# Optimization experiments

Hardware: AMD Instinct MI355X
Metric: run time of the kernel (lower is better)

Reference implementation:

```python
import jax, jax.numpy as jnp
import numpy as np

B, N, D = 8, 1024, 256
H, U = 8, 64  # num_heads, units per head


def setup_inputs() -> dict:
    key = jax.random.key(0)
    ks = jax.random.split(key, 8)
    X = jax.random.normal(ks[0], (B, N, D), dtype=jnp.float32)
    A = (jax.random.uniform(ks[1], (B, N, N)) < 0.1).astype(jnp.float32)
    A = jnp.maximum(A, jnp.eye(N, dtype=jnp.float32)[None])
    s = 1.0 / np.sqrt(D)
    kernel = jax.random.normal(ks[2], (D, H * U), dtype=jnp.float32) * s
    kernel_residual = jax.random.normal(ks[3], (D, H * U), dtype=jnp.float32) * s
    su = 1.0 / np.sqrt(U)
    attn_kernel_self = jax.random.normal(ks[4], (H, U, 1), dtype=jnp.float32) * su
    attn_kernel_neighs = jax.random.normal(ks[5], (H, U, 1), dtype=jnp.float32) * su
    bias = jnp.zeros((H * U,), dtype=jnp.float32)
    return {
        "X": X, "A": A,
        "kernel": kernel, "kernel_residual": kernel_residual,
        "attn_kernel_self": attn_kernel_self,
        "attn_kernel_neighs": attn_kernel_neighs,
        "bias": bias,
    }


def reference(X, A, kernel, kernel_residual, attn_kernel_self, attn_kernel_neighs, bias):
    # feature projections: [B,N,H*U]
    features = X @ kernel
    features_residual = X @ kernel_residual
    f = features.reshape(B, N, H, U)  # bnhu
    # additive attention logits per head
    attn_self = jnp.einsum('bnhu,hu->bnh', f, attn_kernel_self[..., 0])
    attn_neigh = jnp.einsum('bnhu,hu->bnh', f, attn_kernel_neighs[..., 0])
    dense = attn_self[:, :, None, :] + attn_neigh[:, None, :, :]  # b n k h
    dense = jax.nn.leaky_relu(dense, negative_slope=0.2)
    # mask non-edges, softmax over neighbor axis k
    dense = dense + (-1e10) * (1.0 - A)[..., None]
    attn_coef = jax.nn.softmax(dense, axis=2)
    # (dropout is identity in inference mode)
    node_features = jnp.einsum('bnkh,bkhu->bnhu', attn_coef, f)
    node_features = node_features.reshape(B, N, H * U) + features_residual + bias
    # head_reduction == 'concat' -> keep [B,N,H*U]
    return jax.nn.relu(node_features)
```

## Files before the change

### kernel.cpp

```cpp
#include <hip/hip_runtime.h>
#include <stdint.h>


typedef __attribute__((ext_vector_type(8))) short short8;
typedef __attribute__((ext_vector_type(4))) float f32x4;

__device__ __forceinline__ unsigned short f32_to_bf16(float f) {
    unsigned int u = __float_as_uint(f);
    u = (u + 0x7fffu + ((u >> 16) & 1u)) >> 16;
    return (unsigned short)u;
}
__device__ __forceinline__ float bf16_to_f32(unsigned short s) {
    return __uint_as_float(((unsigned int)s) << 16);
}
__device__ __forceinline__ void load_lds16(const unsigned short* g, unsigned short* l) {
    __builtin_amdgcn_global_load_lds(
        (const __attribute__((address_space(1))) unsigned int*)g,
        (__attribute__((address_space(3))) unsigned int*)l, 16, 0, 0);
}

__global__ __launch_bounds__(256) void pack_a(const float* __restrict__ X,
                                              unsigned short* __restrict__ Abig) {
    const int idx = blockIdx.x * 256 + threadIdx.x;
    const int m  = idx >> 6;
    const int kg = (idx & 63) << 2;
    float4 x = *(const float4*)&X[m * 256 + kg];
    const float xs[4] = {x.x, x.y, x.z, x.w};
    union { unsigned short u[4]; uint64_t q; } hq, lq;
    #pragma unroll
    for (int i = 0; i < 4; i++) {
        unsigned short h = f32_to_bf16(xs[i]);
        hq.u[i] = h;
        lq.u[i] = f32_to_bf16(xs[i] - bf16_to_f32(h));
    }
    unsigned short* r = Abig + (size_t)m * 768;
    *(uint64_t*)(r + kg)       = hq.q;
    *(uint64_t*)(r + 256 + kg) = hq.q;
    *(uint64_t*)(r + 512 + kg) = lq.q;
}

__global__ __launch_bounds__(256) void pack_b(const float* __restrict__ Wk,
                                              const float* __restrict__ Wr,
                                              unsigned short* __restrict__ Bpack) {
    const int idx = blockIdx.x * 256 + threadIdx.x;
    const int n = idx / 768;
    const int k = idx - n * 768;
    const float* __restrict__ W = (n < 512) ? Wk : Wr;
    const int nc = n & 511;
    const float w = W[(k & 255) * 512 + nc];
    unsigned short h = f32_to_bf16(w);
    unsigned short o = (k >= 256 && k < 512) ? f32_to_bf16(w - bf16_to_f32(h)) : h;
    Bpack[idx] = o;
}

__global__ __launch_bounds__(512) void attn_ck(const float* __restrict__ kernel,
                                               const float* __restrict__ aks,
                                               const float* __restrict__ akn,
                                               float* __restrict__ ck) {
    const int d = blockIdx.x, j = threadIdx.x;
    const float kv = kernel[d * 512 + j];
    float a = kv * aks[j];
    float b = kv * akn[j];
    #pragma unroll
    for (int m = 32; m; m >>= 1) { a += __shfl_xor(a, m, 64); b += __shfl_xor(b, m, 64); }
    const int lane = j & 63, h = j >> 6;
    if (lane == 0) { ck[d * 16 + h] = a; ck[d * 16 + 8 + h] = b; }
}

__global__ __launch_bounds__(256) void attn_sa(const float* __restrict__ X,
                                               const float* __restrict__ ck,
                                               float* __restrict__ saan) {
    __shared__ __align__(16) float Xs[16][260];
    __shared__ __align__(16) float ckL[4096];
    const int t = threadIdx.x, row0 = blockIdx.x * 16;
    #pragma unroll
    for (int i = 0; i < 4; i++) {
        const int q = t + i * 256;
        const int r = q >> 6, c4 = (q & 63) * 4;
        *(float4*)&Xs[r][c4] = *(const float4*)&X[(size_t)(row0 + r) * 256 + c4];
        *(float4*)&ckL[q * 4] = *(const float4*)&ck[q * 4];
    }
    __syncthreads();
    const int r = t >> 4, o = t & 15;
    float acc = 0.f;
    #pragma unroll 4
    for (int d = 0; d < 256; d++) acc = fmaf(Xs[r][d], ckL[d * 16 + o], acc);
    saan[(size_t)(row0 + r) * 16 + o] = acc;
}

#define GK 768
__global__ __launch_bounds__(256) void gemm_bf16(const unsigned short* __restrict__ Ab,
                                                 const unsigned short* __restrict__ Bp,
                                                 unsigned short* __restrict__ featT,
                                                 float* __restrict__ outr) {
    __shared__ __align__(16) unsigned short As[128 * 32];
    __shared__ __align__(16) unsigned short Bs[128 * 32];
    const int tid = threadIdx.x;
    const int lane = tid & 63, wave = tid >> 6;
    const int wr = wave >> 1, wc = wave & 1;
    const int m0 = blockIdx.x * 128, n0 = blockIdx.y * 128;
    const int l15 = lane & 15, lhi = lane >> 4;

    f32x4 acc[4][4] = {};

    for (int k0 = 0; k0 < GK; k0 += 32) {
        #pragma unroll
        for (int i = 0; i < 2; i++) {
            const int s = tid + i * 256;
            const int row = s >> 2, kc = (s & 3) * 8;
            load_lds16(Ab + (size_t)(m0 + row) * GK + k0 + kc, &As[s * 8]);
            load_lds16(Bp + (size_t)(n0 + row) * GK + k0 + kc, &Bs[s * 8]);
        }
        asm volatile("s_waitcnt vmcnt(0)" ::: "memory");
        __syncthreads();
        short8 a[4], b[4];
        #pragma unroll
        for (int mi = 0; mi < 4; mi++)
            a[mi] = *(const short8*)&As[(wr * 64 + mi * 16 + l15) * 32 + lhi * 8];
        #pragma unroll
        for (int ni = 0; ni < 4; ni++)
            b[ni] = *(const short8*)&Bs[(wc * 64 + ni * 16 + l15) * 32 + lhi * 8];
        #pragma unroll
        for (int mi = 0; mi < 4; mi++)
            #pragma unroll
            for (int ni = 0; ni < 4; ni++)
                acc[mi][ni] = __builtin_amdgcn_mfma_f32_16x16x32_bf16(a[mi], b[ni], acc[mi][ni], 0, 0, 0);
        __syncthreads();
    }

    if (n0 < 512) {
        #pragma unroll
        for (int mi = 0; mi < 4; mi++)
            #pragma unroll
            for (int ni = 0; ni < 4; ni++) {
                const int col = n0 + wc * 64 + ni * 16 + l15;
                const int rbase = m0 + wr * 64 + mi * 16 + lhi * 4;
                const int bb = rbase >> 10, nl = rbase & 1023;
                union { unsigned short u[4]; uint64_t q; } pk;
                #pragma unroll
                for (int r = 0; r < 4; r++) pk.u[r] = f32_to_bf16(acc[mi][ni][r]);
                *(uint64_t*)&featT[(size_t)bb * 524288 + (size_t)col * 1024 + nl] = pk.q;
            }
    } else {
        #pragma unroll
        for (int mi = 0; mi < 4; mi++)
            #pragma unroll
            for (int ni = 0; ni < 4; ni++) {
                const int col = (n0 - 512) + wc * 64 + ni * 16 + l15;
                const int rbase = m0 + wr * 64 + mi * 16 + lhi * 4;
                #pragma unroll
                for (int r = 0; r < 4; r++)
                    outr[(size_t)(rbase + r) * 512 + col] = acc[mi][ni][r];
            }
    }
}

__global__ __launch_bounds__(512) void gat_mfma(
    const float* __restrict__ A, const unsigned short* __restrict__ featT,
    const float* __restrict__ saan, const float* __restrict__ bias,
    float* __restrict__ out) {
    __shared__ float an_s[1024][9];
    __shared__ float A_lds[32][33];
    __shared__ float inv_lds[8][32];

    const int blk = blockIdx.x;
    const int b  = blk & 7;
    const int n0 = (blk >> 3) * 32;
    const int t = threadIdx.x;
    const int w = t >> 6;
    const int lane = t & 63;
    const int l15 = lane & 15, lhi = lane >> 4;

    #pragma unroll
    for (int i = 0; i < 4; i++) {
        const int idx = i * 512 + t;
        const int k = idx >> 1, half = (idx & 1) * 4;
        float4 v = *(const float4*)&saan[(size_t)(b * 1024 + k) * 16 + 8 + half];
        an_s[k][half + 0] = v.x; an_s[k][half + 1] = v.y;
        an_s[k][half + 2] = v.z; an_s[k][half + 3] = v.w;
    }
    float as_r[2];
    #pragma unroll
    for (int mi = 0; mi < 2; mi++)
        as_r[mi] = saan[(size_t)(b * 1024 + n0 + mi * 16 + l15) * 16 + w];

    float4 regA;
    const int sr = t >> 3, sc = (t & 7) * 4;
    if (t < 256)
        regA = *(const float4*)&A[(size_t)(b * 1024 + n0 + sr) * 1024 + sc];

    f32x4 acc[2][4] = {};
    float ps[2] = {0.f, 0.f};
    const unsigned short* __restrict__ fT = featT + (size_t)b * 524288;

    __syncthreads();

    for (int k0 = 0; k0 < 1024; k0 += 32) {
        if (t < 256) {
            A_lds[sr][sc + 0] = regA.x; A_lds[sr][sc + 1] = regA.y;
            A_lds[sr][sc + 2] = regA.z; A_lds[sr][sc + 3] = regA.w;
            if (k0 + 32 < 1024)
                regA = *(const float4*)&A[(size_t)(b * 1024 + n0 + sr) * 1024 + (k0 + 32) + sc];
        }
        __syncthreads();

        union { short8 s8; unsigned int u32[4]; } pa[2];
        #pragma unroll
        for (int mi = 0; mi < 2; mi++) {
            #pragma unroll
            for (int q = 0; q < 4; q++) {
                float pv[2];
                #pragma unroll
                for (int d = 0; d < 2; d++) {
                    const int kk = lhi * 8 + q * 2 + d;
                    float x = as_r[mi] + an_s[k0 + kk][w];
                    x = fmaxf(x, 0.2f * x);
                    const float e = __expf(x);
                    pv[d] = (A_lds[mi * 16 + l15][kk] > 0.5f) ? e : 0.f;
                }
                unsigned int pk;
                asm("v_cvt_pk_bf16_f32 %0, %1, %2" : "=v"(pk) : "v"(pv[0]), "v"(pv[1]));
                pa[mi].u32[q] = pk;
                ps[mi] += __uint_as_float(pk << 16) + __uint_as_float(pk & 0xffff0000u);
            }
        }
        short8 bf[4];
        #pragma unroll
        for (int ni = 0; ni < 4; ni++)
            bf[ni] = *(const short8*)&fT[(size_t)(w * 64 + ni * 16 + l15) * 1024 + k0 + lhi * 8];
        #pragma unroll
        for (int mi = 0; mi < 2; mi++)
            #pragma unroll
            for (int ni = 0; ni < 4; ni++)
                acc[mi][ni] = __builtin_amdgcn_mfma_f32_16x16x32_bf16(pa[mi].s8, bf[ni], acc[mi][ni], 0, 0, 0);
        __syncthreads();
    }

    #pragma unroll
    for (int mi = 0; mi < 2; mi++) {
        ps[mi] += __shfl_xor(ps[mi], 16, 64);
        ps[mi] += __shfl_xor(ps[mi], 32, 64);
        if (lhi == 0) inv_lds[w][mi * 16 + l15] = 1.0f / ps[mi];
    }
    __syncthreads();

    #pragma unroll
    for (int mi = 0; mi < 2; mi++)
        #pragma unroll
        for (int r = 0; r < 4; r++) {
            const int row_l = mi * 16 + lhi * 4 + r;
            const float iv = inv_lds[w][row_l];
            const size_t rb = (size_t)(b * 1024 + n0 + row_l) * 512 + w * 64;
            #pragma unroll
            for (int ni = 0; ni < 4; ni++) {
                const int col = ni * 16 + l15;
                const float v = fmaf(acc[mi][ni][r], iv, out[rb + col] + bias[w * 64 + col]);
                out[rb + col] = fmaxf(v, 0.f);
            }
        }
}

extern "C" void kernel_launch(void* const* d_in, const int* in_sizes, int n_in,
                              void* d_out, int out_size, void* d_ws, size_t ws_size,
                              hipStream_t stream) {
    const float* X    = (const float*)d_in[0];
    const float* A    = (const float*)d_in[1];
    const float* Wk   = (const float*)d_in[2];
    const float* Wr   = (const float*)d_in[3];
    const float* aks  = (const float*)d_in[4];
    const float* akn  = (const float*)d_in[5];
    const float* bias = (const float*)d_in[6];
    float* out = (float*)d_out;

    unsigned short* featT = (unsigned short*)d_ws;
    float* saan = (float*)(featT + (size_t)8 * 512 * 1024);
    float* ck   = saan + (size_t)8192 * 16;
    unsigned short* Abig  = (unsigned short*)(ck + 4096);
    unsigned short* Bpack = Abig + (size_t)8192 * 768;

    pack_a<<<2048, 256, 0, stream>>>(X, Abig);
    pack_b<<<3072, 256, 0, stream>>>(Wk, Wr, Bpack);
    attn_ck<<<256, 512, 0, stream>>>(Wk, aks, akn, ck);
    attn_sa<<<512, 256, 0, stream>>>(X, ck, saan);
    gemm_bf16<<<dim3(64, 8), 256, 0, stream>>>(Abig, Bpack, featT, out);
    gat_mfma<<<256, 512, 0, stream>>>(A, featT, saan, bias, out);
}
```

Before: 183.4 us.

## Shrink GAT tile to 16 rows, read adjacency directly, compute row sums via MFMA

The attention-aggregation kernel now handles 16 query rows per block instead of 32 and launches twice as many blocks. Each lane loads its adjacency values straight from global memory instead of staging them through LDS, which removes the two block barriers per k-step. The softmax denominator is now produced by an extra MFMA against a vector of bf16 ones instead of scalar adds followed by shuffle reductions. In exchange, each block reuses every feature tile for half as many rows, so featT is read twice as often, and the adjacency loads are strided per row.

```diff
diff --git a/kernel.cpp b/kernel.cpp
--- a/kernel.cpp
+++ b/kernel.cpp
@@ -160,12 +160,10 @@
     const float* __restrict__ saan, const float* __restrict__ bias,
     float* __restrict__ out) {
     __shared__ float an_s[1024][9];
-    __shared__ float A_lds[32][33];
-    __shared__ float inv_lds[8][32];
 
     const int blk = blockIdx.x;
     const int b  = blk & 7;
-    const int n0 = (blk >> 3) * 32;
+    const int n0 = (blk >> 3) * 16;
     const int t = threadIdx.x;
     const int w = t >> 6;
     const int lane = t & 63;
@@ -179,85 +177,62 @@
         an_s[k][half + 0] = v.x; an_s[k][half + 1] = v.y;
         an_s[k][half + 2] = v.z; an_s[k][half + 3] = v.w;
     }
-    float as_r[2];
-    #pragma unroll
-    for (int mi = 0; mi < 2; mi++)
-        as_r[mi] = saan[(size_t)(b * 1024 + n0 + mi * 16 + l15) * 16 + w];
-
-    float4 regA;
-    const int sr = t >> 3, sc = (t & 7) * 4;
-    if (t < 256)
-        regA = *(const float4*)&A[(size_t)(b * 1024 + n0 + sr) * 1024 + sc];
-
-    f32x4 acc[2][4] = {};
-    float ps[2] = {0.f, 0.f};
+    const float as_r = saan[(size_t)(b * 1024 + n0 + l15) * 16 + w];
+
+    short8 ones;
+    #pragma unroll
+    for (int i = 0; i < 8; i++) ones[i] = (short)0x3F80;
+
+    f32x4 acc[4] = {};
+    f32x4 accs = {};
     const unsigned short* __restrict__ fT = featT + (size_t)b * 524288;
+    const float* __restrict__ Arow = A + (size_t)(b * 1024 + n0 + l15) * 1024;
 
     __syncthreads();
 
     for (int k0 = 0; k0 < 1024; k0 += 32) {
-        if (t < 256) {
-            A_lds[sr][sc + 0] = regA.x; A_lds[sr][sc + 1] = regA.y;
-            A_lds[sr][sc + 2] = regA.z; A_lds[sr][sc + 3] = regA.w;
-            if (k0 + 32 < 1024)
-                regA = *(const float4*)&A[(size_t)(b * 1024 + n0 + sr) * 1024 + (k0 + 32) + sc];
-        }
-        __syncthreads();
-
-        union { short8 s8; unsigned int u32[4]; } pa[2];
-        #pragma unroll
-        for (int mi = 0; mi < 2; mi++) {
-            #pragma unroll
-            for (int q = 0; q < 4; q++) {
-                float pv[2];
-                #pragma unroll
-                for (int d = 0; d < 2; d++) {
-                    const int kk = lhi * 8 + q * 2 + d;
-                    float x = as_r[mi] + an_s[k0 + kk][w];
-                    x = fmaxf(x, 0.2f * x);
-                    const float e = __expf(x);
-                    pv[d] = (A_lds[mi * 16 + l15][kk] > 0.5f) ? e : 0.f;
-                }
-                unsigned int pk;
-                asm("v_cvt_pk_bf16_f32 %0, %1, %2" : "=v"(pk) : "v"(pv[0]), "v"(pv[1]));
-                pa[mi].u32[q] = pk;
-                ps[mi] += __uint_as_float(pk << 16) + __uint_as_float(pk & 0xffff0000u);
+        float4 a0 = *(const float4*)&Arow[k0 + lhi * 8];
+        float4 a1 = *(const float4*)&Arow[k0 + lhi * 8 + 4];
+        const float av[8] = {a0.x, a0.y, a0.z, a0.w, a1.x, a1.y, a1.z, a1.w};
+
+        union { short8 s8; unsigned int u32[4]; } pa;
+        #pragma unroll
+        for (int q = 0; q < 4; q++) {
+            float pv[2];
+            #pragma unroll
+            for (int d = 0; d < 2; d++) {
+                const int j = q * 2 + d;
+                float x = as_r + an_s[k0 + lhi * 8 + j][w];
+                x = fmaxf(x, 0.2f * x);
+                const float e = __expf(x);
+                pv[d] = (av[j] > 0.5f) ? e : 0.f;
             }
+            unsigned int pk;
+            asm("v_cvt_pk_bf16_f32 %0, %1, %2" : "=v"(pk) : "v"(pv[0]), "v"(pv[1]));
+            pa.u32[q] = pk;
         }
         short8 bf[4];
         #pragma unroll
         for (int ni = 0; ni < 4; ni++)
             bf[ni] = *(const short8*)&fT[(size_t)(w * 64 + ni * 16 + l15) * 1024 + k0 + lhi * 8];
         #pragma unroll
-        for (int mi = 0; mi < 2; mi++)
-            #pragma unroll
-            for (int ni = 0; ni < 4; ni++)
-                acc[mi][ni] = __builtin_amdgcn_mfma_f32_16x16x32_bf16(pa[mi].s8, bf[ni], acc[mi][ni], 0, 0, 0);
-        __syncthreads();
-    }
-
-    #pragma unroll
-    for (int mi = 0; mi < 2; mi++) {
-        ps[mi] += __shfl_xor(ps[mi], 16, 64);
-        ps[mi] += __shfl_xor(ps[mi], 32, 64);
-        if (lhi == 0) inv_lds[w][mi * 16 + l15] = 1.0f / ps[mi];
-    }
-    __syncthreads();
-
-    #pragma unroll
-    for (int mi = 0; mi < 2; mi++)
-        #pragma unroll
-        for (int r = 0; r < 4; r++) {
-            const int row_l = mi * 16 + lhi * 4 + r;
-            const float iv = inv_lds[w][row_l];
-            const size_t rb = (size_t)(b * 1024 + n0 + row_l) * 512 + w * 64;
-            #pragma unroll
-            for (int ni = 0; ni < 4; ni++) {
-                const int col = ni * 16 + l15;
-                const float v = fmaf(acc[mi][ni][r], iv, out[rb + col] + bias[w * 64 + col]);
-                out[rb + col] = fmaxf(v, 0.f);
-            }
+        for (int ni = 0; ni < 4; ni++)
+            acc[ni] = __builtin_amdgcn_mfma_f32_16x16x32_bf16(pa.s8, bf[ni], acc[ni], 0, 0, 0);
+        accs = __builtin_amdgcn_mfma_f32_16x16x32_bf16(pa.s8, ones, accs, 0, 0, 0);
+    }
+
+    #pragma unroll
+    for (int r = 0; r < 4; r++) {
+        const int row_l = lhi * 4 + r;
+        const float iv = 1.0f / accs[r];
+        const size_t rb = (size_t)(b * 1024 + n0 + row_l) * 512 + w * 64;
+        #pragma unroll
+        for (int ni = 0; ni < 4; ni++) {
+            const int col = ni * 16 + l15;
+            const float v = fmaf(acc[ni][r], iv, out[rb + col] + bias[w * 64 + col]);
+            out[rb + col] = fmaxf(v, 0.f);
         }
+    }
 }
 
 extern "C" void kernel_launch(void* const* d_in, const int* in_sizes, int n_in,
@@ -283,5 +258,5 @@
     attn_ck<<<256, 512, 0, stream>>>(Wk, aks, akn, ck);
     attn_sa<<<512, 256, 0, stream>>>(X, ck, saan);
     gemm_bf16<<<dim3(64, 8), 256, 0, stream>>>(Abig, Bpack, featT, out);
-    gat_mfma<<<256, 512, 0, stream>>>(A, featT, saan, bias, out);
-}
+    gat_mfma<<<512, 512, 0, stream>>>(A, featT, saan, bias, out);
+}
```

New measurement: 218.2 us. 19.0% more time.
